# Performance work log

Hardware: AMD Instinct MI355X
Metric: run time of the kernel (lower is better)

The kernel has to match this reference:

```python
import jax, jax.numpy as jnp
import numpy as np

DIM = 64   # flow dimension
HID = 8    # hidden_dim=[8]
B = 131072 # batch of samples


def setup_inputs() -> dict:
    key = jax.random.key(0)
    ks = jax.random.split(key, 6)
    L = DIM - 1  # number of per-dim MLPs (layers[0..L-1], layer l has fan-in l+1)
    lim = float(np.sqrt(0.5))
    x = jax.random.normal(ks[0], (B, DIM), jnp.float32)
    initial_param = jax.random.uniform(ks[1], (2,), jnp.float32, -lim, lim)
    # Ragged Linear(fan_in=l+1, 8) weights stacked into padded [L, HID, L];
    # entries beyond column l are masked to zero in reference().
    fan_in = np.arange(1, DIM).astype(np.float32)          # (L,)
    bnd1 = (1.0 / np.sqrt(fan_in))[:, None, None]          # torch Linear default init bound
    W1 = jax.random.uniform(ks[2], (L, HID, L), jnp.float32, -1.0, 1.0) * bnd1
    b1 = jax.random.uniform(ks[3], (L, HID), jnp.float32, -1.0, 1.0) * bnd1[:, :, 0]
    bnd2 = 1.0 / np.sqrt(HID)
    W2 = jax.random.uniform(ks[4], (L, 2, HID), jnp.float32, -bnd2, bnd2)
    b2 = jax.random.uniform(ks[5], (L, 2), jnp.float32, -bnd2, bnd2)
    return {"x": x, "initial_param": initial_param, "W1": W1, "b1": b1, "W2": W2, "b2": b2}


def reference(x, initial_param, W1, b1, W2, b2):
    B_, D = x.shape
    L = W1.shape[0]  # D - 1
    # mask[l, d] = 1 iff d <= l  ->  layer l sees exactly x[:, :l+1]
    mask = jnp.tril(jnp.ones((L, L), x.dtype))
    W1m = W1 * mask[:, None, :]
    # all dim-1 tiny MLPs fused into two batched contractions
    h = jnp.tanh(jnp.einsum('bd,lhd->blh', x[:, :L], W1m) + b1)   # [B, L, HID]
    out = jnp.einsum('blh,loh->blo', h, W2) + b2                   # [B, L, 2]
    mu0 = jnp.broadcast_to(initial_param[0], (B_, 1)).astype(x.dtype)
    al0 = jnp.broadcast_to(initial_param[1], (B_, 1)).astype(x.dtype)
    mu = jnp.concatenate([mu0, out[:, :, 0]], axis=1)              # [B, D]
    alpha = jnp.concatenate([al0, out[:, :, 1]], axis=1)           # [B, D]
    z = x * jnp.exp(alpha) + mu
    log_det = jnp.sum(alpha, axis=1)
    return z, log_det
```

## Files before the change

kernel.cpp:

```cpp
#include <hip/hip_runtime.h>


#define DIMS 64
#define TPB  1024
#define WAVES 16
#define SPW  16

typedef __attribute__((ext_vector_type(8))) short short8;
typedef __attribute__((ext_vector_type(4))) float f32x4;
typedef __attribute__((ext_vector_type(4))) unsigned int uint4v;
typedef unsigned short ushort_t;
typedef unsigned int uint_t;

#if __has_builtin(__builtin_amdgcn_exp2f)
#define YSCALE 2.8853900817779268f
#define EXPY(x) __builtin_amdgcn_exp2f(x)
#define EXP2F(x) __builtin_amdgcn_exp2f(x)
#else
#define YSCALE 2.0f
#define EXPY(x) __expf(x)
#define EXP2F(x) exp2f(x)
#endif
#define LOG2E 1.4426950408889634f

#define A_OFF 0
#define B_OFF 16384
#define C_OFF 49152
#define D_OFF 53248
#define E_OFF 55296
#define WT_BYTES 55808
#define WT_CHUNKS (WT_BYTES / 16)
#define XZ_OFF WT_BYTES
#define LDS_BYTES (WT_BYTES + WAVES * SPW * DIMS * 4)
#define PREP_N (24576 + 1664)

__device__ __align__(16) unsigned char g_ws[WT_BYTES];

__device__ __forceinline__ uint_t pk2bf(float a, float b) {
#if __has_builtin(__builtin_amdgcn_cvt_pk_bf16_f32)
    typedef __attribute__((ext_vector_type(2))) __bf16 bf16x2;
    bf16x2 r = __builtin_amdgcn_cvt_pk_bf16_f32(a, b);
    return __builtin_bit_cast(uint_t, r);
#else
    uint_t ua = __float_as_uint(a); ua += 0x7FFFu + ((ua >> 16) & 1u);
    uint_t ub = __float_as_uint(b); ub += 0x7FFFu + ((ub >> 16) & 1u);
    return (ub & 0xFFFF0000u) | (ua >> 16);
#endif
}

__device__ __forceinline__ ushort_t f2bf(float f) {
    uint_t u = __float_as_uint(f);
    u += 0x7FFFu + ((u >> 16) & 1u);
    return (ushort_t)(u >> 16);
}

__device__ __forceinline__ int logrow(int p) {
    int n = p & 15;
    return (p >> 5) * 32 + (n >> 2) * 8 + ((p >> 4) & 1) * 4 + (n & 3);
}

__global__ void siaf_prep(const float* __restrict__ W1, const float* __restrict__ b1,
                          const float* __restrict__ W2, const float* __restrict__ b2) {
    ushort_t* __restrict__ ws_u = (ushort_t*)g_ws;
    int i = blockIdx.x * 256 + threadIdx.x;
    if (i < 8192) {
        int p = i >> 5, e = i & 31;
        int cp = e >> 3, j = e & 7;
        int k = ((cp ^ (p & 3)) << 3) | j;
        int L = logrow(p), l = L >> 3, h = L & 7;
        float v = (k <= l) ? W1[(l * 8 + h) * 63 + k] * YSCALE : 0.0f;
        ws_u[i] = f2bf(v);
    } else if (i < 24576) {
        int v_ = i - 8192;
        int p = 256 + (v_ >> 6), e = v_ & 63;
        int cp = e >> 3, j = e & 7;
        int k = ((cp ^ (p & 7)) << 3) | j;
        int L = logrow(p), l = L >> 3, h = L & 7;
        float v = (l < 63 && k <= l) ? W1[(l * 8 + h) * 63 + k] * YSCALE : 0.0f;
        ws_u[i] = f2bf(v);
    } else if (i < PREP_N) {
        int f = i - 24576;
        float* fws = (float*)(ws_u + 24576);
        float v = 0.0f;
        if (f < 1024) {
            int l = f >> 4, o = (f >> 3) & 1, h = f & 7;
            if (l < 63) v = W2[(l * 2 + o) * 8 + h];
        } else if (f < 1536) {
            int p = f - 1024;
            int L = logrow(p), l = L >> 3, h = L & 7;
            if (l < 63) v = b1[l * 8 + h] * YSCALE;
        } else {
            int j = f - 1536, l = j >> 1, o = j & 1;
            if (l < 63) v = b2[l * 2 + o];
        }
        fws[f] = v;
    }
}

__device__ __forceinline__ float th(float t) {
    float e = EXPY(t);
    float r = __builtin_amdgcn_rcpf(e + 1.0f);
    return fmaf(-2.0f, r, 1.0f);
}

__global__ __launch_bounds__(TPB, 4) void siaf_main(
        const float* __restrict__ x, const float* __restrict__ ip,
        float* __restrict__ out, int nB) {
    extern __shared__ unsigned char lds[];

    const int tid  = threadIdx.x;
    const int wv   = tid >> 6, lane = tid & 63;
    const int s16  = lane & 15, quad = lane >> 4;
    const int sbase = blockIdx.x * (WAVES * SPW) + wv * SPW;
    float* xzw = (float*)(lds + XZ_OFF) + wv * (SPW * DIMS);

    #pragma unroll
    for (int g = 0; g < 4; ++g) {
        const float4 v = ((const float4*)(x + (size_t)sbase * DIMS))[g * 64 + lane];
        const int s_loc = 4 * g + quad;
        const int pc = (s16 ^ s_loc) & 15;
        *(float4*)(xzw + s_loc * 64 + pc * 4) = v;
    }
    const float ip0 = ip[0], ip1 = ip[1];

    {
        const uint4* __restrict__ wsv = (const uint4*)g_ws;
        uint4* dst = (uint4*)lds;
        for (int c = tid; c < WT_CHUNKS; c += TPB) dst[c] = wsv[c];
    }

    short8 bfr[2];
    #pragma unroll
    for (int kh = 0; kh < 2; ++kh) {
        const int c0 = kh * 8 + quad * 2;
        float4 va = *(const float4*)(xzw + s16 * 64 + ((c0 ^ s16) & 15) * 4);
        float4 vb = *(const float4*)(xzw + s16 * 64 + (((c0 + 1) ^ s16) & 15) * 4);
        uint4v u = {pk2bf(va.x, va.y), pk2bf(va.z, va.w),
                    pk2bf(vb.x, vb.y), pk2bf(vb.z, vb.w)};
        bfr[kh] = __builtin_bit_cast(short8, u);
    }

    __syncthreads();

    const ushort_t* wA  = (const ushort_t*)(lds + A_OFF);
    const ushort_t* wB  = (const ushort_t*)(lds + B_OFF);
    const float*    w2f = (const float*)(lds + C_OFF);
    const float*    b1f = (const float*)(lds + D_OFF);
    const float*    b2f = (const float*)(lds + E_OFF);

    auto ldfr = [&](int w, short8& a00, short8& a10, short8& a01, short8& a11) {
        if (w < 8) {
            const ushort_t* base = wA + (w * 32 + s16) * 32;
            const int pc = quad ^ (s16 & 3);
            a00 = *(const short8*)(base + pc * 8);
            a10 = *(const short8*)(base + 512 + pc * 8);
        } else {
            const ushort_t* base = wB + ((w - 8) * 32 + s16) * 64;
            const int pc = quad ^ (s16 & 7);
            a00 = *(const short8*)(base + pc * 8);
            a10 = *(const short8*)(base + 1024 + pc * 8);
            a01 = *(const short8*)(base + (pc ^ 4) * 8);
            a11 = *(const short8*)(base + 1024 + (pc ^ 4) * 8);
        }
    };
    auto ldbi = [&](int w, float4& bi0, float4& bi1) {
        bi0 = *(const float4*)(b1f + w * 32 + quad * 4);
        bi1 = *(const float4*)(b1f + w * 32 + 16 + quad * 4);
    };

    short8 A00[2], A10[2], A01[2] = {}, A11[2] = {};
    float4 BI0[2], BI1[2];
    ldfr(0, A00[0], A10[0], A01[0], A11[0]);
    ldbi(0, BI0[0], BI1[0]);

    float lsum = 0.0f;
    #pragma unroll
    for (int w = 0; w < 16; ++w) {
        const int cur = w & 1, nxt = cur ^ 1;

        const int l = 4 * w + quad;
        const float4 m0 = *(const float4*)(w2f + l * 16);
        const float4 m1 = *(const float4*)(w2f + l * 16 + 4);
        const float4 a0 = *(const float4*)(w2f + l * 16 + 8);
        const float4 a1 = *(const float4*)(w2f + l * 16 + 12);
        const float2 bb = *(const float2*)(b2f + l * 2);

        if (w < 15) {
            ldfr(w + 1, A00[nxt], A10[nxt], A01[nxt], A11[nxt]);
            ldbi(w + 1, BI0[nxt], BI1[nxt]);
        }

        f32x4 aE = {BI0[cur].x, BI0[cur].y, BI0[cur].z, BI0[cur].w};
        f32x4 aO = {BI1[cur].x, BI1[cur].y, BI1[cur].z, BI1[cur].w};
        aE = __builtin_amdgcn_mfma_f32_16x16x32_bf16(A00[cur], bfr[0], aE, 0, 0, 0);
        aO = __builtin_amdgcn_mfma_f32_16x16x32_bf16(A10[cur], bfr[0], aO, 0, 0, 0);
        if (w >= 8) {
            aE = __builtin_amdgcn_mfma_f32_16x16x32_bf16(A01[cur], bfr[1], aE, 0, 0, 0);
            aO = __builtin_amdgcn_mfma_f32_16x16x32_bf16(A11[cur], bfr[1], aO, 0, 0, 0);
        }

        const float t0 = th(aE[0]), t1 = th(aE[1]), t2 = th(aE[2]), t3 = th(aE[3]);
        const float t4 = th(aO[0]), t5 = th(aO[1]), t6 = th(aO[2]), t7 = th(aO[3]);

        float mu0 = bb.x, mu1 = m1.x * t4;
        mu0 = fmaf(m0.x, t0, mu0); mu1 = fmaf(m1.y, t5, mu1);
        mu0 = fmaf(m0.y, t1, mu0); mu1 = fmaf(m1.z, t6, mu1);
        mu0 = fmaf(m0.z, t2, mu0); mu1 = fmaf(m1.w, t7, mu1);
        mu0 = fmaf(m0.w, t3, mu0);
        const float mu = mu0 + mu1;
        float al0 = bb.y, al1 = a1.x * t4;
        al0 = fmaf(a0.x, t0, al0); al1 = fmaf(a1.y, t5, al1);
        al0 = fmaf(a0.y, t1, al0); al1 = fmaf(a1.z, t6, al1);
        al0 = fmaf(a0.z, t2, al0); al1 = fmaf(a1.w, t7, al1);
        al0 = fmaf(a0.w, t3, al0);
        const float al = al0 + al1;

        const bool pad = (l == 63);
        const float alB = pad ? ip1 : al;
        const float muB = pad ? ip0 : mu;
        const int d = pad ? 0 : (l + 1);
        float* pz = xzw + s16 * 64 + ((((d >> 2) ^ s16) & 15) << 2) + (d & 3);
        *pz = fmaf(*pz, EXP2F(alB * LOG2E), muB);
        lsum += alB;
    }

    #pragma unroll
    for (int g = 0; g < 4; ++g) {
        const int s_loc = 4 * g + quad;
        const int pc = (s16 ^ s_loc) & 15;
        const float4 v = *(const float4*)(xzw + s_loc * 64 + pc * 4);
        ((float4*)(out + (size_t)sbase * DIMS))[g * 64 + lane] = v;
    }

    {
        float v = lsum;
        int r1 = __builtin_amdgcn_ds_swizzle(__float_as_int(v), 0x401F);
        v += __int_as_float(r1);
        int r2 = __builtin_amdgcn_ds_bpermute((lane ^ 32) << 2, __float_as_int(v));
        v += __int_as_float(r2);
        if (quad == 0)
            out[(size_t)nB * DIMS + sbase + s16] = v;
    }
}

extern "C" void kernel_launch(void* const* d_in, const int* in_sizes, int n_in,
                              void* d_out, int out_size, void* d_ws, size_t ws_size,
                              hipStream_t stream) {
    const float* x  = (const float*)d_in[0];
    const float* ip = (const float*)d_in[1];
    const float* W1 = (const float*)d_in[2];
    const float* b1 = (const float*)d_in[3];
    const float* W2 = (const float*)d_in[4];
    const float* b2 = (const float*)d_in[5];
    float* out = (float*)d_out;
    (void)d_ws; (void)ws_size;

    const int nB = in_sizes[0] / DIMS;

    (void)hipFuncSetAttribute((const void*)siaf_main,
                              hipFuncAttributeMaxDynamicSharedMemorySize, LDS_BYTES);

    siaf_prep<<<(PREP_N + 255) / 256, 256, 0, stream>>>(W1, b1, W2, b2);
    siaf_main<<<nB / (WAVES * SPW), TPB, LDS_BYTES, stream>>>(x, ip, out, nB);
}
```

Before: 114.2 us.

## Load MFMA weight fragments directly from global memory instead of staging in LDS

```diff
diff --git a/kernel.cpp b/kernel.cpp
--- a/kernel.cpp
+++ b/kernel.cpp
@@ -2,8 +2,8 @@
 
 
 #define DIMS 64
-#define TPB  1024
-#define WAVES 16
+#define TPB  512
+#define WAVES 8
 #define SPW  16
 
 typedef __attribute__((ext_vector_type(8))) short short8;
@@ -24,15 +24,15 @@
 #define LOG2E 1.4426950408889634f
 
 #define A_OFF 0
-#define B_OFF 16384
+#define BLO_OFF 16384
+#define BHI_OFF 32768
 #define C_OFF 49152
-#define D_OFF 53248
-#define E_OFF 55296
 #define WT_BYTES 55808
-#define WT_CHUNKS (WT_BYTES / 16)
-#define XZ_OFF WT_BYTES
-#define LDS_BYTES (WT_BYTES + WAVES * SPW * DIMS * 4)
+#define CDE_BYTES 6656
 #define PREP_N (24576 + 1664)
+
+#define XZ_OFF CDE_BYTES
+#define LDS_BYTES (CDE_BYTES + WAVES * SPW * DIMS * 4)
 
 __device__ __align__(16) unsigned char g_ws[WT_BYTES];
 
@@ -64,17 +64,19 @@
     ushort_t* __restrict__ ws_u = (ushort_t*)g_ws;
     int i = blockIdx.x * 256 + threadIdx.x;
     if (i < 8192) {
-        int p = i >> 5, e = i & 31;
-        int cp = e >> 3, j = e & 7;
-        int k = ((cp ^ (p & 3)) << 3) | j;
+        int p = i >> 5, k = i & 31;
         int L = logrow(p), l = L >> 3, h = L & 7;
         float v = (k <= l) ? W1[(l * 8 + h) * 63 + k] * YSCALE : 0.0f;
         ws_u[i] = f2bf(v);
+    } else if (i < 16384) {
+        int r = i - 8192;
+        int p = 256 + (r >> 5), k = r & 31;
+        int L = logrow(p), l = L >> 3, h = L & 7;
+        float v = (l < 63 && k <= l) ? W1[(l * 8 + h) * 63 + k] * YSCALE : 0.0f;
+        ws_u[i] = f2bf(v);
     } else if (i < 24576) {
-        int v_ = i - 8192;
-        int p = 256 + (v_ >> 6), e = v_ & 63;
-        int cp = e >> 3, j = e & 7;
-        int k = ((cp ^ (p & 7)) << 3) | j;
+        int r = i - 16384;
+        int p = 256 + (r >> 5), k = 32 + (r & 31);
         int L = logrow(p), l = L >> 3, h = L & 7;
         float v = (l < 63 && k <= l) ? W1[(l * 8 + h) * 63 + k] * YSCALE : 0.0f;
         ws_u[i] = f2bf(v);
@@ -103,7 +105,7 @@
     return fmaf(-2.0f, r, 1.0f);
 }
 
-__global__ __launch_bounds__(TPB, 4) void siaf_main(
+__global__ __launch_bounds__(TPB, 8) void siaf_main(
         const float* __restrict__ x, const float* __restrict__ ip,
         float* __restrict__ out, int nB) {
     extern __shared__ unsigned char lds[];
@@ -123,10 +125,8 @@
     }
     const float ip0 = ip[0], ip1 = ip[1];
 
-    {
-        const uint4* __restrict__ wsv = (const uint4*)g_ws;
-        uint4* dst = (uint4*)lds;
-        for (int c = tid; c < WT_CHUNKS; c += TPB) dst[c] = wsv[c];
+    if (tid < CDE_BYTES / 16) {
+        ((uint4*)lds)[tid] = ((const uint4*)(g_ws + C_OFF))[tid];
     }
 
     short8 bfr[2];
@@ -142,41 +142,53 @@
 
     __syncthreads();
 
-    const ushort_t* wA  = (const ushort_t*)(lds + A_OFF);
-    const ushort_t* wB  = (const ushort_t*)(lds + B_OFF);
-    const float*    w2f = (const float*)(lds + C_OFF);
-    const float*    b1f = (const float*)(lds + D_OFF);
-    const float*    b2f = (const float*)(lds + E_OFF);
-
-    auto ldfr = [&](int w, short8& a00, short8& a10, short8& a01, short8& a11) {
+    const float* w2f = (const float*)(lds);
+    const float* b1f = (const float*)(lds + 4096);
+    const float* b2f = (const float*)(lds + 6144);
+
+    const ushort_t* gA   = (const ushort_t*)g_ws;
+    const ushort_t* gBlo = (const ushort_t*)(g_ws + BLO_OFF);
+    const ushort_t* gBhi = (const ushort_t*)(g_ws + BHI_OFF);
+    const int fo = s16 * 32 + quad * 8;
+
+    auto ldA = [&](int w, short8& a00, short8& a10, short8& a01, short8& a11) {
         if (w < 8) {
-            const ushort_t* base = wA + (w * 32 + s16) * 32;
-            const int pc = quad ^ (s16 & 3);
-            a00 = *(const short8*)(base + pc * 8);
-            a10 = *(const short8*)(base + 512 + pc * 8);
+            const ushort_t* b = gA + w * 1024 + fo;
+            a00 = *(const short8*)(b);
+            a10 = *(const short8*)(b + 512);
         } else {
-            const ushort_t* base = wB + ((w - 8) * 32 + s16) * 64;
-            const int pc = quad ^ (s16 & 7);
-            a00 = *(const short8*)(base + pc * 8);
-            a10 = *(const short8*)(base + 1024 + pc * 8);
-            a01 = *(const short8*)(base + (pc ^ 4) * 8);
-            a11 = *(const short8*)(base + 1024 + (pc ^ 4) * 8);
+            const int off = (w - 8) * 1024 + fo;
+            a00 = *(const short8*)(gBlo + off);
+            a10 = *(const short8*)(gBlo + off + 512);
+            a01 = *(const short8*)(gBhi + off);
+            a11 = *(const short8*)(gBhi + off + 512);
         }
     };
-    auto ldbi = [&](int w, float4& bi0, float4& bi1) {
-        bi0 = *(const float4*)(b1f + w * 32 + quad * 4);
-        bi1 = *(const float4*)(b1f + w * 32 + 16 + quad * 4);
-    };
 
     short8 A00[2], A10[2], A01[2] = {}, A11[2] = {};
-    float4 BI0[2], BI1[2];
-    ldfr(0, A00[0], A10[0], A01[0], A11[0]);
-    ldbi(0, BI0[0], BI1[0]);
+    ldA(0, A00[0], A10[0], A01[0], A11[0]);
 
     float lsum = 0.0f;
     #pragma unroll
     for (int w = 0; w < 16; ++w) {
         const int cur = w & 1, nxt = cur ^ 1;
+
+        if (w < 15) ldA(w + 1, A00[nxt], A10[nxt], A01[nxt], A11[nxt]);
+
+        const float4 bi0 = *(const float4*)(b1f + w * 32 + quad * 4);
+        const float4 bi1 = *(const float4*)(b1f + w * 32 + 16 + quad * 4);
+
+        f32x4 aE = {bi0.x, bi0.y, bi0.z, bi0.w};
+        f32x4 aO = {bi1.x, bi1.y, bi1.z, bi1.w};
+        aE = __builtin_amdgcn_mfma_f32_16x16x32_bf16(A00[cur], bfr[0], aE, 0, 0, 0);
+        aO = __builtin_amdgcn_mfma_f32_16x16x32_bf16(A10[cur], bfr[0], aO, 0, 0, 0);
+        if (w >= 8) {
+            aE = __builtin_amdgcn_mfma_f32_16x16x32_bf16(A01[cur], bfr[1], aE, 0, 0, 0);
+            aO = __builtin_amdgcn_mfma_f32_16x16x32_bf16(A11[cur], bfr[1], aO, 0, 0, 0);
+        }
+
+        const float t0 = th(aE[0]), t1 = th(aE[1]), t2 = th(aE[2]), t3 = th(aE[3]);
+        const float t4 = th(aO[0]), t5 = th(aO[1]), t6 = th(aO[2]), t7 = th(aO[3]);
 
         const int l = 4 * w + quad;
         const float4 m0 = *(const float4*)(w2f + l * 16);
@@ -184,23 +196,6 @@
         const float4 a0 = *(const float4*)(w2f + l * 16 + 8);
         const float4 a1 = *(const float4*)(w2f + l * 16 + 12);
         const float2 bb = *(const float2*)(b2f + l * 2);
-
-        if (w < 15) {
-            ldfr(w + 1, A00[nxt], A10[nxt], A01[nxt], A11[nxt]);
-            ldbi(w + 1, BI0[nxt], BI1[nxt]);
-        }
-
-        f32x4 aE = {BI0[cur].x, BI0[cur].y, BI0[cur].z, BI0[cur].w};
-        f32x4 aO = {BI1[cur].x, BI1[cur].y, BI1[cur].z, BI1[cur].w};
-        aE = __builtin_amdgcn_mfma_f32_16x16x32_bf16(A00[cur], bfr[0], aE, 0, 0, 0);
-        aO = __builtin_amdgcn_mfma_f32_16x16x32_bf16(A10[cur], bfr[0], aO, 0, 0, 0);
-        if (w >= 8) {
-            aE = __builtin_amdgcn_mfma_f32_16x16x32_bf16(A01[cur], bfr[1], aE, 0, 0, 0);
-            aO = __builtin_amdgcn_mfma_f32_16x16x32_bf16(A11[cur], bfr[1], aO, 0, 0, 0);
-        }
-
-        const float t0 = th(aE[0]), t1 = th(aE[1]), t2 = th(aE[2]), t3 = th(aE[3]);
-        const float t4 = th(aO[0]), t5 = th(aO[1]), t6 = th(aO[2]), t7 = th(aO[3]);
 
         float mu0 = bb.x, mu1 = m1.x * t4;
         mu0 = fmaf(m0.x, t0, mu0); mu1 = fmaf(m1.y, t5, mu1);
```

Measured after the change: 114.0 us. Within noise of the previous version (-0.2%).
